# Performance work log

Measured on AMD Instinct MI355X. Metric: run time of the kernel, lower is better.

## Reference

```python
import jax, jax.numpy as jnp
import numpy as np

D_MODEL = 256
D_INNER = 512    # expand=2
D_STATE = 16
D_CONV = 4
DT_RANK = 16     # ceil(256/16)
N_BLOCKS = 4
EPS = 1e-5


def setup_inputs() -> dict:
    key = jax.random.key(0)
    ks = jax.random.split(key, 8)
    s = 0.02
    return {
        "x": jax.random.normal(ks[0], (1, 4, D_MODEL, 32, 32), jnp.float32),
        "norm_w": jnp.ones((N_BLOCKS, D_MODEL), jnp.float32),
        "norm_b": jnp.zeros((N_BLOCKS, D_MODEL), jnp.float32),
        "in_w": jax.random.normal(ks[1], (N_BLOCKS, 2 * D_INNER, D_MODEL), jnp.float32) * s,
        "conv_w": jax.random.normal(ks[2], (N_BLOCKS, D_INNER, D_CONV), jnp.float32) * s,
        "conv_b": jnp.zeros((N_BLOCKS, D_INNER), jnp.float32),
        "xproj_w": jax.random.normal(ks[3], (N_BLOCKS, DT_RANK + 2 * D_STATE, D_INNER), jnp.float32) * s,
        "dtproj_w": jax.random.normal(ks[4], (N_BLOCKS, D_INNER, DT_RANK), jnp.float32) * s,
        "dtproj_b": jax.random.normal(ks[5], (N_BLOCKS, D_INNER), jnp.float32) * s,
        "A_log": jnp.tile(jnp.log(jnp.arange(1, D_STATE + 1, dtype=jnp.float32))[None, None, :],
                          (N_BLOCKS, D_INNER, 1)),
        "Dp": jnp.ones((N_BLOCKS, D_INNER), jnp.float32),
        "out_w": jax.random.normal(ks[6], (N_BLOCKS, D_MODEL, D_INNER), jnp.float32) * s,
    }


def _layernorm(x, w, b):
    mu = jnp.mean(x, axis=-1, keepdims=True)
    var = jnp.var(x, axis=-1, keepdims=True)
    return (x - mu) / jnp.sqrt(var + EPS) * w + b


def _mamba(h, in_w, conv_w, conv_b, xproj_w, dtproj_w, dtproj_b, A_log, Dp, out_w):
    # h: (B, L, d_model)
    B, L, _ = h.shape
    xz = h @ in_w.T                                   # (B, L, 2*d_inner)
    x, z = jnp.split(xz, 2, axis=-1)
    # causal depthwise conv1d, kernel size D_CONV
    xp = jnp.pad(x, ((0, 0), (D_CONV - 1, 0), (0, 0)))
    xc = sum(xp[:, k:k + L, :] * conv_w[:, k] for k in range(D_CONV)) + conv_b
    x = jax.nn.silu(xc)                               # (B, L, d_inner)
    dbl = x @ xproj_w.T                               # (B, L, dt_rank + 2*d_state)
    dt = dbl[..., :DT_RANK]
    Bm = dbl[..., DT_RANK:DT_RANK + D_STATE]          # (B, L, n)
    Cm = dbl[..., DT_RANK + D_STATE:]                 # (B, L, n)
    dt = jax.nn.softplus(dt @ dtproj_w.T + dtproj_b)  # (B, L, d_inner)
    A = -jnp.exp(A_log)                               # (d_inner, n)
    dA = jnp.exp(dt[..., None] * A)                   # (B, L, d_inner, n)
    dBx = dt[..., None] * Bm[:, :, None, :] * x[..., None]

    def step(hprev, inp):
        dA_t, dBx_t, C_t = inp
        hcur = dA_t * hprev + dBx_t                   # (B, d_inner, n)
        return hcur, jnp.einsum('bdn,bn->bd', hcur, C_t)

    h0 = jnp.zeros((B, D_INNER, D_STATE), x.dtype)
    _, y = jax.lax.scan(step, h0, (dA.transpose(1, 0, 2, 3),
                                   dBx.transpose(1, 0, 2, 3),
                                   Cm.transpose(1, 0, 2)))
    y = y.transpose(1, 0, 2)                          # (B, L, d_inner)
    y = (y + Dp * x) * jax.nn.silu(z)
    return y @ out_w.T                                # (B, L, d_model)


def _forward(x, norm_w, norm_b, in_w, conv_w, conv_b, xproj_w, dtproj_w, dtproj_b, A_log, Dp, out_w):
    b, n, c, h, w = x.shape
    hs = x.reshape(b * n, c, h * w).transpose(0, 2, 1)  # (bn, hw, c)

    def blk(i, hidden, resid):
        resid = hidden if resid is None else resid + hidden
        hn = _layernorm(resid, norm_w[i], norm_b[i])
        out = _mamba(hn, in_w[i], conv_w[i], conv_b[i], xproj_w[i],
                     dtproj_w[i], dtproj_b[i], A_log[i], Dp[i], out_w[i])
        return out, resid

    res = None
    for i in range(2):  # pairs of (forward, backward-flipped) blocks
        hf, rf = blk(2 * i, hs, res)
        hb, rb = blk(2 * i + 1, hs[:, ::-1], None if res is None else res[:, ::-1])
        hs = hf + hb[:, ::-1]
        res = rf + rb[:, ::-1]
    res = res + hs
    return res.transpose(0, 2, 1).reshape(b, n, c, h, w)


def reference(x, norm_w, norm_b, in_w, conv_w, conv_b, xproj_w, dtproj_w, dtproj_b, A_log, Dp, out_w):
    return _forward(x, norm_w, norm_b, in_w, conv_w, conv_b, xproj_w,
                    dtproj_w, dtproj_b, A_log, Dp, out_w)
```

## Files before the change

kernel.cpp:

```cpp
#include <hip/hip_runtime.h>
#include <math.h>


__device__ __forceinline__ float sigmoidf_(float x){ return 1.f/(1.f+__expf(-x)); }
__device__ __forceinline__ short bf16_(float x){
  unsigned u = __float_as_uint(x);
  u += 0x7FFFu + ((u>>16)&1u);
  return (short)(u>>16);
}
__device__ __forceinline__ float f32_(short s){
  return __uint_as_float(((unsigned)(unsigned short)s)<<16);
}

using fragAB = __attribute__((ext_vector_type(8))) short;
using fragC  = __attribute__((ext_vector_type(4))) float;

__global__ __launch_bounds__(256) void k_transpose_in(const float* __restrict__ x, float* __restrict__ hs){
  __shared__ float tile[32][33];
  int b = blockIdx.z;
  int l0 = blockIdx.x*32, c0 = blockIdx.y*32;
  int tx = threadIdx.x, ty = threadIdx.y;
  #pragma unroll
  for (int j=0;j<32;j+=8)
    tile[ty+j][tx] = x[(size_t)b*262144 + (size_t)(c0+ty+j)*1024 + l0 + tx];
  __syncthreads();
  #pragma unroll
  for (int j=0;j<32;j+=8)
    hs[(size_t)b*262144 + (size_t)(l0+ty+j)*256 + (c0+tx)] = tile[tx][ty+j];
}

__global__ __launch_bounds__(256) void k_final(const float* __restrict__ racc, const float* __restrict__ hs, float* __restrict__ out){
  __shared__ float tile[32][33];
  int b = blockIdx.z;
  int l0 = blockIdx.x*32, c0 = blockIdx.y*32;
  int tx = threadIdx.x, ty = threadIdx.y;
  #pragma unroll
  for (int j=0;j<32;j+=8){
    size_t idx = (size_t)b*262144 + (size_t)(l0+ty+j)*256 + c0+tx;
    tile[ty+j][tx] = 2.f*racc[idx] + hs[idx];
  }
  __syncthreads();
  #pragma unroll
  for (int j=0;j<32;j+=8)
    out[(size_t)b*262144 + (size_t)(c0+ty+j)*1024 + l0+tx] = tile[tx][ty+j];
}

__global__ __launch_bounds__(256) void k_ln(const float* __restrict__ hs, float* __restrict__ racc, short* __restrict__ hn_f,
  const float* __restrict__ nw, const float* __restrict__ nb, int layer0, int first){
  int row = blockIdx.x, c = threadIdx.x;
  size_t idx = (size_t)row*256 + c;
  float r = hs[idx];
  if (!first) r += 2.f*racc[idx];
  racc[idx] = r;
  float s1=r, s2=r*r;
  #pragma unroll
  for (int o=32;o>=1;o>>=1){ s1+=__shfl_xor(s1,o); s2+=__shfl_xor(s2,o); }
  __shared__ float red[8];
  int wid=c>>6, lane=c&63;
  if (lane==0){ red[wid]=s1; red[4+wid]=s2; }
  __syncthreads();
  s1 = red[0]+red[1]+red[2]+red[3];
  s2 = red[4]+red[5]+red[6]+red[7];
  float mu = s1*(1.f/256.f);
  float var = s2*(1.f/256.f) - mu*mu;
  float inv = rsqrtf(var + 1e-5f);
  float nv = (r-mu)*inv;
  size_t fo = (((size_t)(row>>4)*32 + (c>>3))*16 + (row&15))*8 + (c&7);
  hn_f[fo]           = bf16_(nv*nw[layer0*256+c] + nb[layer0*256+c]);
  hn_f[1048576 + fo] = bf16_(nv*nw[(layer0+1)*256+c] + nb[(layer0+1)*256+c]);
}

__global__ __launch_bounds__(256) void k_wconv(
  const float* __restrict__ inw, const float* __restrict__ xpw,
  const float* __restrict__ dtw, const float* __restrict__ otw,
  short* __restrict__ f_inw, short* __restrict__ f_xpw,
  short* __restrict__ f_dtw, short* __restrict__ f_otw,
  short* __restrict__ dt_f)
{
  int which = blockIdx.y, layer = blockIdx.z;
  int idx = blockIdx.x*256 + threadIdx.x;
  if (which==4){
    if (layer) return;
    if (idx >= 131072) return;
    int st = idx >> 16, rem = idx & 65535;
    int mt = rem >> 8, kt2 = (rem>>7)&1, e = rem&127;
    dt_f[(size_t)st*131072 + ((size_t)(mt*4 + 2 + kt2))*128 + e] = 0;
    return;
  }
  const float* src; short* dst; int R,K,Kp;
  if (which==0){ src=inw; dst=f_inw; R=1024; K=256; Kp=256; }
  else if (which==1){ src=xpw; dst=f_xpw; R=48; K=512; Kp=512; }
  else if (which==2){ src=dtw; dst=f_dtw; R=512; K=16; Kp=32; }
  else { src=otw; dst=f_otw; R=256; K=512; Kp=512; }
  int per = (R>>4)*(Kp>>3)*128;
  if (idx >= per) return;
  int e = idx & 127, tile = idx >> 7;
  int nkt = Kp>>3;
  int kt = tile % nkt, rt = tile / nkt;
  int r = rt*16 + (e>>3), k = kt*8 + (e&7);
  float v = (k<K) ? src[((size_t)layer*R + r)*K + k] : 0.f;
  dst[(size_t)layer*per + idx] = bf16_(v);
}

__global__ __launch_bounds__(256) void k_mm(
  const short* __restrict__ Af, long sA,
  const short* __restrict__ Wf, long sW,
  const short* __restrict__ A2f, const short* __restrict__ W2f,
  float* __restrict__ Cb, long sC,
  const float* __restrict__ biasb, long sBias,
  int M, int N, int K, int ldc, int mode,
  short* __restrict__ aux1, long sAux1,
  short* __restrict__ aux2, long sAux2)
{
  int z = blockIdx.z;
  int tid = threadIdx.x;
  int lane = tid & 63, wid = tid >> 6;
  int wm = wid & 1, wn = wid >> 1;
  int K8 = K >> 3;
  int mt_base = blockIdx.y*8 + wm*4;
  int nt_base = blockIdx.x*4 + wn*2;
  int ncap = (N + 15) >> 4;
  const int loff = lane*8;
  fragC acc[4][2] = {};
  const short* Aps[2] = { Af + (size_t)z*sA, A2f };
  const short* Wps[2] = { Wf + (size_t)z*sW, W2f };
  int nseg = A2f ? 2 : 1;
  for (int sgi=0; sgi<nseg; ++sgi){
    const short* A = Aps[sgi];
    const short* W = Wps[sgi];
    for (int kt=0; kt<K8; kt+=4){
      fragAB a[4], b[2];
      #pragma unroll
      for (int i=0;i<4;++i)
        a[i] = *(const fragAB*)(A + ((size_t)(mt_base+i)*K8 + kt)*128 + loff);
      #pragma unroll
      for (int j=0;j<2;++j){
        int nt = nt_base + j; if (nt >= ncap) nt = ncap-1;
        b[j] = *(const fragAB*)(W + ((size_t)nt*K8 + kt)*128 + loff);
      }
      #pragma unroll
      for (int i=0;i<4;++i)
        #pragma unroll
        for (int j=0;j<2;++j)
          acc[i][j] = __builtin_amdgcn_mfma_f32_16x16x32_bf16(a[i], b[j], acc[i][j], 0,0,0);
    }
  }
  float* C = Cb ? Cb + (size_t)z*sC : nullptr;
  const float* bias = biasb ? biasb + (size_t)z*sBias : nullptr;
  int r0 = (lane>>4)*4;
  int cc = lane & 15;
  #pragma unroll
  for (int i=0;i<4;++i){
    int row = (mt_base+i)*16 + r0;
    #pragma unroll
    for (int j=0;j<2;++j){
      int col = (nt_base+j)*16 + cc;
      if (col < N){
        #pragma unroll
        for (int r=0;r<4;++r){
          float v = acc[i][j][r];
          if (bias) v += bias[col];
          if (mode==2){ v = (v > 20.f) ? v : log1pf(__expf(v)); }
          int rr = row + r;
          if (mode==3){
            if (col < 512) aux1[(size_t)z*sAux1 + (size_t)rr*512 + col] = bf16_(v);
            else           aux2[(size_t)z*sAux2 + (size_t)rr*512 + (col-512)] = bf16_(v);
          } else {
            C[(size_t)rr*ldc + col] = v;
            if (mode==1 && col < 16)
              aux1[(size_t)z*sAux1 + (((size_t)(rr>>4)*4 + (col>>3))*16 + (rr&15))*8 + (col&7)] = bf16_(v);
          }
        }
      }
    }
  }
}

__global__ __launch_bounds__(256) void k_conv(const short* __restrict__ xb, short* __restrict__ xc_f,
  const float* __restrict__ cw, const float* __restrict__ cb, int layer0){
  int idx = blockIdx.x*256 + threadIdx.x;
  int d = idx & 511;
  int t = (idx >> 9) & 1023;
  int sb = idx >> 19;
  int s = sb >> 2, b = sb & 3;
  int layer = layer0 + s;
  const float* w = cw + ((size_t)layer*512 + d)*4;
  float accv = cb[(size_t)layer*512 + d];
  const short* xp = xb + (size_t)s*2097152 + (size_t)b*1024*512 + d;
  if (s==0){
    #pragma unroll
    for (int k=0;k<4;++k){ int tt = t + k - 3; if (tt>=0) accv = fmaf(f32_(xp[(size_t)tt*512]), w[k], accv); }
  } else {
    #pragma unroll
    for (int k=0;k<4;++k){ int tt = t + 3 - k; if (tt<1024) accv = fmaf(f32_(xp[(size_t)tt*512]), w[k], accv); }
  }
  float v = accv * sigmoidf_(accv);
  int row = b*1024 + t;
  xc_f[(size_t)s*2097152 + (((size_t)(row>>4)*64 + (d>>3))*16 + (row&15))*8 + (d&7)] = bf16_(v);
}

#define NCHUNK 64
#define CSTEPS 16

__device__ __forceinline__ float ld_xc(const short* xcf, int row, int d){
  return f32_(xcf[(((size_t)(row>>4)*64 + (d>>3))*16 + (row&15))*8 + (d&7)]);
}

__global__ __launch_bounds__(256) void k_scan_a(
  const float* __restrict__ dtv, const short* __restrict__ xc_f,
  const float* __restrict__ dbl, const float* __restrict__ A_log,
  float* __restrict__ dtsum, float* __restrict__ hF, int layer0)
{
  int d = blockIdx.x*256 + threadIdx.x;
  int k = blockIdx.y;
  int sb = blockIdx.z;
  int s = sb >> 2, b = sb & 3;
  int layer = layer0 + s;
  float Av[16];
  #pragma unroll
  for (int n=0;n<16;++n) Av[n] = -__expf(A_log[((size_t)layer*512 + d)*16 + n]);
  const float* dt_p = dtv + (size_t)sb*524288 + d;
  const short* xcf = xc_f + (size_t)s*2097152;
  const float* bc_p = dbl + (size_t)sb*49152;
  float h[16];
  #pragma unroll
  for (int n=0;n<16;++n) h[n] = 0.f;
  float ssum = 0.f;
  int u0 = k*CSTEPS;
  #pragma unroll
  for (int i=0;i<CSTEPS;++i){
    int u = u0 + i;
    int t = s ? (1023 - u) : u;
    int row = b*1024 + t;
    float dtval = dt_p[(size_t)t*512];
    float xv = ld_xc(xcf, row, d);
    const float4* bp = (const float4*)(bc_p + (size_t)t*48 + 16);
    float4 B0 = bp[0], B1 = bp[1], B2 = bp[2], B3 = bp[3];
    float Bv[16] = {B0.x,B0.y,B0.z,B0.w,B1.x,B1.y,B1.z,B1.w,
                    B2.x,B2.y,B2.z,B2.w,B3.x,B3.y,B3.z,B3.w};
    float w = dtval * xv;
    ssum += dtval;
    #pragma unroll
    for (int n=0;n<16;++n)
      h[n] = fmaf(__expf(dtval*Av[n]), h[n], w*Bv[n]);
  }
  size_t base = (size_t)(sb*NCHUNK + k)*512 + d;
  dtsum[base] = ssum;
  float4* hp = (float4*)(hF + base*16);
  #pragma unroll
  for (int q=0;q<4;++q) hp[q] = make_float4(h[4*q],h[4*q+1],h[4*q+2],h[4*q+3]);
}

__global__ __launch_bounds__(256) void k_scan_c(
  const float* __restrict__ dtsum, float* __restrict__ hF,
  const float* __restrict__ A_log, int layer0)
{
  int gid = blockIdx.x*256 + threadIdx.x;
  int sb = gid >> 13;
  int d = (gid >> 4) & 511;
  int n = gid & 15;
  int layer = layer0 + (sb >> 2);
  float Av = -__expf(A_log[((size_t)layer*512 + d)*16 + n]);
  float hrun = 0.f;
  #pragma unroll 8
  for (int k=0;k<NCHUNK;++k){
    size_t base = (size_t)(sb*NCHUNK + k)*512 + d;
    float a = __expf(Av * dtsum[base]);
    float hf = hF[base*16 + n];
    hF[base*16 + n] = hrun;
    hrun = fmaf(a, hrun, hf);
  }
}

__global__ __launch_bounds__(256) void k_scan_b(
  const float* __restrict__ dtv, const short* __restrict__ xc_f, const short* __restrict__ zb,
  const float* __restrict__ dbl, const float* __restrict__ A_log, const float* __restrict__ Dp,
  const float* __restrict__ h0p, short* __restrict__ y_f, int layer0)
{
  int d = blockIdx.x*256 + threadIdx.x;
  int k = blockIdx.y;
  int sb = blockIdx.z;
  int s = sb >> 2, b = sb & 3;
  int layer = layer0 + s;
  float Av[16];
  #pragma unroll
  for (int n=0;n<16;++n) Av[n] = -__expf(A_log[((size_t)layer*512 + d)*16 + n]);
  float Dv = Dp[(size_t)layer*512 + d];
  const float* dt_p = dtv + (size_t)sb*524288 + d;
  const short* xcf = xc_f + (size_t)s*2097152;
  const short* z_p = zb + (size_t)s*2097152 + (size_t)b*1024*512 + d;
  const float* bc_p = dbl + (size_t)sb*49152;
  size_t base = (size_t)(sb*NCHUNK + k)*512 + d;
  float h[16];
  const float4* hp = (const float4*)(h0p + base*16);
  #pragma unroll
  for (int q=0;q<4;++q){
    float4 v = hp[q];
    h[4*q]=v.x; h[4*q+1]=v.y; h[4*q+2]=v.z; h[4*q+3]=v.w;
  }
  short* yo = y_f + (size_t)s*2097152;
  int u0 = k*CSTEPS;
  #pragma unroll
  for (int i=0;i<CSTEPS;++i){
    int u = u0 + i;
    int t = s ? (1023 - u) : u;
    int row = b*1024 + t;
    float dtval = dt_p[(size_t)t*512];
    float xv = ld_xc(xcf, row, d);
    const float4* bp = (const float4*)(bc_p + (size_t)t*48 + 16);
    float4 B0 = bp[0], B1 = bp[1], B2 = bp[2], B3 = bp[3];
    float4 C0 = bp[4], C1 = bp[5], C2 = bp[6], C3 = bp[7];
    float Bv[16] = {B0.x,B0.y,B0.z,B0.w,B1.x,B1.y,B1.z,B1.w,
                    B2.x,B2.y,B2.z,B2.w,B3.x,B3.y,B3.z,B3.w};
    float Cv[16] = {C0.x,C0.y,C0.z,C0.w,C1.x,C1.y,C1.z,C1.w,
                    C2.x,C2.y,C2.z,C2.w,C3.x,C3.y,C3.z,C3.w};
    float w = dtval * xv;
    float y = 0.f;
    #pragma unroll
    for (int n=0;n<16;++n){
      h[n] = fmaf(__expf(dtval*Av[n]), h[n], w*Bv[n]);
      y = fmaf(h[n], Cv[n], y);
    }
    float zv = f32_(z_p[(size_t)t*512]);
    float yv = (y + Dv*xv) * (zv*sigmoidf_(zv));
    yo[(((size_t)(row>>4)*64 + (d>>3))*16 + (row&15))*8 + (d&7)] = bf16_(yv);
  }
}

extern "C" void kernel_launch(void* const* d_in, const int* in_sizes, int n_in,
                              void* d_out, int out_size, void* d_ws, size_t ws_size,
                              hipStream_t stream) {
  const float* x        = (const float*)d_in[0];
  const float* norm_w   = (const float*)d_in[1];
  const float* norm_b   = (const float*)d_in[2];
  const float* in_w     = (const float*)d_in[3];
  const float* conv_w   = (const float*)d_in[4];
  const float* conv_b   = (const float*)d_in[5];
  const float* xproj_w  = (const float*)d_in[6];
  const float* dtproj_w = (const float*)d_in[7];
  const float* dtproj_b = (const float*)d_in[8];
  const float* A_log    = (const float*)d_in[9];
  const float* Dp       = (const float*)d_in[10];
  const float* out_w    = (const float*)d_in[11];
  float* out = (float*)d_out;
  float* ws = (float*)d_ws;

  float* hs    = ws;
  float* racc  = ws + 1048576;
  short* hn_f  = (short*)(ws + 2097152);
  short* xb    = (short*)(ws + 3145728);
  short* zb    = (short*)(ws + 5242880);
  short* xc_f  = (short*)(ws + 7340032);
  short* y_f   = (short*)(ws + 9437184);
  float* dbl   = ws + 11534336;
  float* dtv   = ws + 12058624;
  short* dt_f  = (short*)(ws + 16252928);
  float* dtsum = ws + 16384000;
  float* hF    = ws + 16646144;
  short* w_inw = (short*)(ws + 20840448);
  short* w_xp  = w_inw + 1048576;
  short* w_dt  = w_xp + 98304;
  short* w_out = w_dt + 65536;

  k_wconv<<<dim3(1024,5,4), 256, 0, stream>>>(in_w, xproj_w, dtproj_w, out_w,
      w_inw, w_xp, w_dt, w_out, dt_f);
  k_transpose_in<<<dim3(32,8,4), dim3(32,8), 0, stream>>>(x, hs);

  for (int it=0; it<2; ++it){
    int layer0 = 2*it;
    k_ln<<<4096, 256, 0, stream>>>(hs, racc, hn_f, norm_w, norm_b, layer0, it==0 ? 1 : 0);
    k_mm<<<dim3(16,32,2), 256, 0, stream>>>(hn_f, 1048576L, w_inw + (size_t)layer0*262144, 262144L,
        nullptr, nullptr, nullptr, 0L, nullptr, 0L, 4096, 1024, 256, 0, 3,
        xb, 2097152L, zb, 2097152L);
    k_conv<<<16384, 256, 0, stream>>>(xb, xc_f, conv_w, conv_b, layer0);
    k_mm<<<dim3(1,32,2), 256, 0, stream>>>(xc_f, 2097152L, w_xp + (size_t)layer0*24576, 24576L,
        nullptr, nullptr, dbl, 196608L, nullptr, 0L, 4096, 48, 512, 48, 1,
        dt_f, 131072L, nullptr, 0L);
    k_mm<<<dim3(8,32,2), 256, 0, stream>>>(dt_f, 131072L, w_dt + (size_t)layer0*16384, 16384L,
        nullptr, nullptr, dtv, 2097152L, dtproj_b + (size_t)layer0*512, 512L, 4096, 512, 32, 512, 2,
        nullptr, 0L, nullptr, 0L);
    k_scan_a<<<dim3(2,NCHUNK,8), 256, 0, stream>>>(dtv, xc_f, dbl, A_log, dtsum, hF, layer0);
    k_scan_c<<<256, 256, 0, stream>>>(dtsum, hF, A_log, layer0);
    k_scan_b<<<dim3(2,NCHUNK,8), 256, 0, stream>>>(dtv, xc_f, zb, dbl, A_log, Dp, hF, y_f, layer0);
    k_mm<<<dim3(4,32,1), 256, 0, stream>>>(y_f, 0L, w_out + (size_t)layer0*131072, 0L,
        y_f + 2097152, w_out + (size_t)(layer0+1)*131072, hs, 0L, nullptr, 0L,
        4096, 256, 512, 256, 0, nullptr, 0L, nullptr, 0L);
  }
  k_final<<<dim3(32,8,4), dim3(32,8), 0, stream>>>(racc, hs, out);
}
```

Before: 458.2 us.

## Fuse x/dt projections, widen GEMM tiles, parallelize chunk scan, compact weight conversion

The x-projection and dt-projection GEMMs are fused into one kernel that keeps the dt slice in LDS and applies bias and softplus in place, so the dt_f round trip and one launch go away. The generic GEMM becomes k_mm4 with 4x4 MFMA tiles per wave, which halves the grid and raises per-wave reuse. The sequential cross-chunk scan in k_scan_c becomes a parallel warp-shuffle prefix scan over chunks per (d, sb) block. Weight conversion uses a compact 1D grid with no idle blocks. In exchange, the larger tiles raise register pressure and the in_proj grid drops to 512 blocks, and the scan now assumes NCHUNK equals 64.

```diff
diff --git a/kernel.cpp b/kernel.cpp
--- a/kernel.cpp
+++ b/kernel.cpp
@@ -74,26 +74,20 @@
   const float* __restrict__ inw, const float* __restrict__ xpw,
   const float* __restrict__ dtw, const float* __restrict__ otw,
   short* __restrict__ f_inw, short* __restrict__ f_xpw,
-  short* __restrict__ f_dtw, short* __restrict__ f_otw,
-  short* __restrict__ dt_f)
-{
-  int which = blockIdx.y, layer = blockIdx.z;
-  int idx = blockIdx.x*256 + threadIdx.x;
-  if (which==4){
-    if (layer) return;
-    if (idx >= 131072) return;
-    int st = idx >> 16, rem = idx & 65535;
-    int mt = rem >> 8, kt2 = (rem>>7)&1, e = rem&127;
-    dt_f[(size_t)st*131072 + ((size_t)(mt*4 + 2 + kt2))*128 + e] = 0;
-    return;
-  }
+  short* __restrict__ f_dtw, short* __restrict__ f_otw)
+{
+  int b = blockIdx.x, tid = threadIdx.x;
+  int which, layer, idx;
+  if (b < 4096){ which=0; layer=b>>10; idx=((b&1023)<<8)+tid; }
+  else if (b < 4480){ int r=b-4096; which=1; layer=r/96;  idx=(r%96)*256+tid; }
+  else if (b < 4736){ int r=b-4480; which=2; layer=r>>6;  idx=(r&63)*256+tid; }
+  else              { int r=b-4736; which=3; layer=r>>9;  idx=(r&511)*256+tid; }
   const float* src; short* dst; int R,K,Kp;
   if (which==0){ src=inw; dst=f_inw; R=1024; K=256; Kp=256; }
   else if (which==1){ src=xpw; dst=f_xpw; R=48; K=512; Kp=512; }
   else if (which==2){ src=dtw; dst=f_dtw; R=512; K=16; Kp=32; }
   else { src=otw; dst=f_otw; R=256; K=512; Kp=512; }
   int per = (R>>4)*(Kp>>3)*128;
-  if (idx >= per) return;
   int e = idx & 127, tile = idx >> 7;
   int nkt = Kp>>3;
   int kt = tile % nkt, rt = tile / nkt;
@@ -102,13 +96,12 @@
   dst[(size_t)layer*per + idx] = bf16_(v);
 }
 
-__global__ __launch_bounds__(256) void k_mm(
+__global__ __launch_bounds__(256) void k_mm4(
   const short* __restrict__ Af, long sA,
   const short* __restrict__ Wf, long sW,
   const short* __restrict__ A2f, const short* __restrict__ W2f,
   float* __restrict__ Cb, long sC,
-  const float* __restrict__ biasb, long sBias,
-  int M, int N, int K, int ldc, int mode,
+  int K, int ldc, int mode,
   short* __restrict__ aux1, long sAux1,
   short* __restrict__ aux2, long sAux2)
 {
@@ -118,10 +111,9 @@
   int wm = wid & 1, wn = wid >> 1;
   int K8 = K >> 3;
   int mt_base = blockIdx.y*8 + wm*4;
-  int nt_base = blockIdx.x*4 + wn*2;
-  int ncap = (N + 15) >> 4;
+  int nt_base = blockIdx.x*8 + wn*4;
   const int loff = lane*8;
-  fragC acc[4][2] = {};
+  fragC acc[4][4] = {};
   const short* Aps[2] = { Af + (size_t)z*sA, A2f };
   const short* Wps[2] = { Wf + (size_t)z*sW, W2f };
   int nseg = A2f ? 2 : 1;
@@ -129,46 +121,125 @@
     const short* A = Aps[sgi];
     const short* W = Wps[sgi];
     for (int kt=0; kt<K8; kt+=4){
-      fragAB a[4], b[2];
+      fragAB a[4], b[4];
       #pragma unroll
       for (int i=0;i<4;++i)
         a[i] = *(const fragAB*)(A + ((size_t)(mt_base+i)*K8 + kt)*128 + loff);
       #pragma unroll
-      for (int j=0;j<2;++j){
-        int nt = nt_base + j; if (nt >= ncap) nt = ncap-1;
-        b[j] = *(const fragAB*)(W + ((size_t)nt*K8 + kt)*128 + loff);
-      }
+      for (int j=0;j<4;++j)
+        b[j] = *(const fragAB*)(W + ((size_t)(nt_base+j)*K8 + kt)*128 + loff);
       #pragma unroll
       for (int i=0;i<4;++i)
         #pragma unroll
-        for (int j=0;j<2;++j)
+        for (int j=0;j<4;++j)
           acc[i][j] = __builtin_amdgcn_mfma_f32_16x16x32_bf16(a[i], b[j], acc[i][j], 0,0,0);
     }
   }
   float* C = Cb ? Cb + (size_t)z*sC : nullptr;
-  const float* bias = biasb ? biasb + (size_t)z*sBias : nullptr;
   int r0 = (lane>>4)*4;
   int cc = lane & 15;
   #pragma unroll
   for (int i=0;i<4;++i){
     int row = (mt_base+i)*16 + r0;
     #pragma unroll
-    for (int j=0;j<2;++j){
+    for (int j=0;j<4;++j){
       int col = (nt_base+j)*16 + cc;
-      if (col < N){
+      #pragma unroll
+      for (int r=0;r<4;++r){
+        float v = acc[i][j][r];
+        int rr = row + r;
+        if (mode==3){
+          if (col < 512) aux1[(size_t)z*sAux1 + (size_t)rr*512 + col] = bf16_(v);
+          else           aux2[(size_t)z*sAux2 + (size_t)rr*512 + (col-512)] = bf16_(v);
+        } else {
+          C[(size_t)rr*ldc + col] = v;
+        }
+      }
+    }
+  }
+}
+
+__global__ __launch_bounds__(256) void k_xpdt(
+  const short* __restrict__ xc_f, const short* __restrict__ wxp,
+  const short* __restrict__ wdt, const float* __restrict__ dtb,
+  float* __restrict__ dbl, float* __restrict__ dtv, int layer0)
+{
+  __shared__ short dt_lds[32][24];
+  int z = blockIdx.y;
+  int by = blockIdx.x;
+  int layer = layer0 + z;
+  int tid = threadIdx.x, lane = tid & 63, wn = tid >> 6;
+  const short* A = xc_f + (size_t)z*2097152;
+  const short* W = wxp + (size_t)layer*24576;
+  int mt0 = by*2;
+  const int loff = lane*8;
+  int r0 = (lane>>4)*4, cc = lane & 15;
+  {
+    fragC acc[2] = {};
+    int nt = wn < 3 ? wn : 2;
+    for (int kt=0; kt<64; kt+=4){
+      fragAB a0 = *(const fragAB*)(A + ((size_t)(mt0+0)*64 + kt)*128 + loff);
+      fragAB a1 = *(const fragAB*)(A + ((size_t)(mt0+1)*64 + kt)*128 + loff);
+      fragAB b  = *(const fragAB*)(W + ((size_t)nt*64 + kt)*128 + loff);
+      acc[0] = __builtin_amdgcn_mfma_f32_16x16x32_bf16(a0, b, acc[0], 0,0,0);
+      acc[1] = __builtin_amdgcn_mfma_f32_16x16x32_bf16(a1, b, acc[1], 0,0,0);
+    }
+    int col = nt*16 + cc;
+    #pragma unroll
+    for (int i=0;i<2;++i){
+      int lr = i*16 + r0;
+      int grow = by*32 + lr;
+      #pragma unroll
+      for (int r=0;r<4;++r){
+        float v = acc[i][r];
+        if (wn==1 || wn==2)
+          dbl[(size_t)z*196608 + (size_t)(grow+r)*48 + col] = v;
+        if (wn==0)
+          dt_lds[lr+r][cc] = bf16_(v);
+      }
+    }
+  }
+  __syncthreads();
+  {
+    float* dto = dtv + (size_t)z*2097152;
+    const float* bias = dtb + (size_t)layer*512;
+    const short* WD = wdt + (size_t)layer*16384;
+    int kq = lane >> 4;
+    fragAB a2[2];
+    #pragma unroll
+    for (int i=0;i<2;++i){
+      fragAB t = {};
+      if (kq < 2){
         #pragma unroll
-        for (int r=0;r<4;++r){
-          float v = acc[i][j][r];
-          if (bias) v += bias[col];
-          if (mode==2){ v = (v > 20.f) ? v : log1pf(__expf(v)); }
-          int rr = row + r;
-          if (mode==3){
-            if (col < 512) aux1[(size_t)z*sAux1 + (size_t)rr*512 + col] = bf16_(v);
-            else           aux2[(size_t)z*sAux2 + (size_t)rr*512 + (col-512)] = bf16_(v);
-          } else {
-            C[(size_t)rr*ldc + col] = v;
-            if (mode==1 && col < 16)
-              aux1[(size_t)z*sAux1 + (((size_t)(rr>>4)*4 + (col>>3))*16 + (rr&15))*8 + (col&7)] = bf16_(v);
+        for (int j=0;j<8;++j) t[j] = dt_lds[i*16 + (lane&15)][kq*8 + j];
+      }
+      a2[i] = t;
+    }
+    #pragma unroll
+    for (int c2=0;c2<2;++c2){
+      fragC acc2[2][4] = {};
+      fragAB b2[4];
+      #pragma unroll
+      for (int j=0;j<4;++j){
+        int ntj = wn*8 + c2*4 + j;
+        b2[j] = *(const fragAB*)(WD + ((size_t)ntj*4)*128 + loff);
+      }
+      #pragma unroll
+      for (int i=0;i<2;++i)
+        #pragma unroll
+        for (int j=0;j<4;++j)
+          acc2[i][j] = __builtin_amdgcn_mfma_f32_16x16x32_bf16(a2[i], b2[j], acc2[i][j], 0,0,0);
+      #pragma unroll
+      for (int i=0;i<2;++i){
+        int grow = by*32 + i*16 + r0;
+        #pragma unroll
+        for (int j=0;j<4;++j){
+          int col2 = (wn*8 + c2*4 + j)*16 + cc;
+          #pragma unroll
+          for (int r=0;r<4;++r){
+            float v = acc2[i][j][r] + bias[col2];
+            v = (v > 20.f) ? v : log1pf(__expf(v));
+            dto[(size_t)(grow+r)*512 + col2] = v;
           }
         }
       }
@@ -255,20 +326,41 @@
   const float* __restrict__ dtsum, float* __restrict__ hF,
   const float* __restrict__ A_log, int layer0)
 {
-  int gid = blockIdx.x*256 + threadIdx.x;
-  int sb = gid >> 13;
-  int d = (gid >> 4) & 511;
-  int n = gid & 15;
+  __shared__ float tile[64][17];
+  __shared__ float ds[64];
+  int d = blockIdx.x, sb = blockIdx.y;
+  int tid = threadIdx.x, lane = tid & 63, w = tid >> 6;
   int layer = layer0 + (sb >> 2);
-  float Av = -__expf(A_log[((size_t)layer*512 + d)*16 + n]);
-  float hrun = 0.f;
-  #pragma unroll 8
-  for (int k=0;k<NCHUNK;++k){
-    size_t base = (size_t)(sb*NCHUNK + k)*512 + d;
-    float a = __expf(Av * dtsum[base]);
-    float hf = hF[base*16 + n];
-    hF[base*16 + n] = hrun;
-    hrun = fmaf(a, hrun, hf);
+  size_t base = (size_t)sb*64*8192 + (size_t)d*16;
+  {
+    int k = tid >> 2, n0 = (tid & 3)*4;
+    float4 v = *(const float4*)(hF + base + (size_t)k*8192 + n0);
+    tile[k][n0+0]=v.x; tile[k][n0+1]=v.y; tile[k][n0+2]=v.z; tile[k][n0+3]=v.w;
+  }
+  if (tid < 64) ds[tid] = dtsum[((size_t)sb*64 + tid)*512 + d];
+  __syncthreads();
+  float dsk = ds[lane];
+  #pragma unroll
+  for (int p=0;p<4;++p){
+    int n = p*4 + w;
+    float Av = -__expf(A_log[((size_t)layer*512 + d)*16 + n]);
+    float a = __expf(Av * dsk);
+    float h = tile[lane][n];
+    #pragma unroll
+    for (int o=1;o<64;o<<=1){
+      float au = __shfl_up(a, o);
+      float hu = __shfl_up(h, o);
+      if (lane >= o){ h = fmaf(a, hu, h); a *= au; }
+    }
+    float h0 = __shfl_up(h, 1);
+    if (lane == 0) h0 = 0.f;
+    tile[lane][n] = h0;
+  }
+  __syncthreads();
+  {
+    int k = tid >> 2, n0 = (tid & 3)*4;
+    float4 v = make_float4(tile[k][n0], tile[k][n0+1], tile[k][n0+2], tile[k][n0+3]);
+    *(float4*)(hF + base + (size_t)k*8192 + n0) = v;
   }
 }
 
@@ -354,37 +446,29 @@
   short* y_f   = (short*)(ws + 9437184);
   float* dbl   = ws + 11534336;
   float* dtv   = ws + 12058624;
-  short* dt_f  = (short*)(ws + 16252928);
-  float* dtsum = ws + 16384000;
-  float* hF    = ws + 16646144;
-  short* w_inw = (short*)(ws + 20840448);
+  float* dtsum = ws + 16252928;
+  float* hF    = ws + 16515072;
+  short* w_inw = (short*)(ws + 20709376);
   short* w_xp  = w_inw + 1048576;
   short* w_dt  = w_xp + 98304;
   short* w_out = w_dt + 65536;
 
-  k_wconv<<<dim3(1024,5,4), 256, 0, stream>>>(in_w, xproj_w, dtproj_w, out_w,
-      w_inw, w_xp, w_dt, w_out, dt_f);
+  k_wconv<<<6784, 256, 0, stream>>>(in_w, xproj_w, dtproj_w, out_w, w_inw, w_xp, w_dt, w_out);
   k_transpose_in<<<dim3(32,8,4), dim3(32,8), 0, stream>>>(x, hs);
 
   for (int it=0; it<2; ++it){
     int layer0 = 2*it;
     k_ln<<<4096, 256, 0, stream>>>(hs, racc, hn_f, norm_w, norm_b, layer0, it==0 ? 1 : 0);
-    k_mm<<<dim3(16,32,2), 256, 0, stream>>>(hn_f, 1048576L, w_inw + (size_t)layer0*262144, 262144L,
-        nullptr, nullptr, nullptr, 0L, nullptr, 0L, 4096, 1024, 256, 0, 3,
-        xb, 2097152L, zb, 2097152L);
+    k_mm4<<<dim3(8,32,2), 256, 0, stream>>>(hn_f, 1048576L, w_inw + (size_t)layer0*262144, 262144L,
+        nullptr, nullptr, nullptr, 0L, 256, 0, 3, xb, 2097152L, zb, 2097152L);
     k_conv<<<16384, 256, 0, stream>>>(xb, xc_f, conv_w, conv_b, layer0);
-    k_mm<<<dim3(1,32,2), 256, 0, stream>>>(xc_f, 2097152L, w_xp + (size_t)layer0*24576, 24576L,
-        nullptr, nullptr, dbl, 196608L, nullptr, 0L, 4096, 48, 512, 48, 1,
-        dt_f, 131072L, nullptr, 0L);
-    k_mm<<<dim3(8,32,2), 256, 0, stream>>>(dt_f, 131072L, w_dt + (size_t)layer0*16384, 16384L,
-        nullptr, nullptr, dtv, 2097152L, dtproj_b + (size_t)layer0*512, 512L, 4096, 512, 32, 512, 2,
+    k_xpdt<<<dim3(128,2), 256, 0, stream>>>(xc_f, w_xp, w_dt, dtproj_b, dbl, dtv, layer0);
+    k_scan_a<<<dim3(2,NCHUNK,8), 256, 0, stream>>>(dtv, xc_f, dbl, A_log, dtsum, hF, layer0);
+    k_scan_c<<<dim3(512,8), 256, 0, stream>>>(dtsum, hF, A_log, layer0);
+    k_scan_b<<<dim3(2,NCHUNK,8), 256, 0, stream>>>(dtv, xc_f, zb, dbl, A_log, Dp, hF, y_f, layer0);
+    k_mm4<<<dim3(2,32,1), 256, 0, stream>>>(y_f, 0L, w_out + (size_t)layer0*131072, 0L,
+        y_f + 2097152, w_out + (size_t)(layer0+1)*131072, hs, 0L, 512, 256, 0,
         nullptr, 0L, nullptr, 0L);
-    k_scan_a<<<dim3(2,NCHUNK,8), 256, 0, stream>>>(dtv, xc_f, dbl, A_log, dtsum, hF, layer0);
-    k_scan_c<<<256, 256, 0, stream>>>(dtsum, hF, A_log, layer0);
-    k_scan_b<<<dim3(2,NCHUNK,8), 256, 0, stream>>>(dtv, xc_f, zb, dbl, A_log, Dp, hF, y_f, layer0);
-    k_mm<<<dim3(4,32,1), 256, 0, stream>>>(y_f, 0L, w_out + (size_t)layer0*131072, 0L,
-        y_f + 2097152, w_out + (size_t)(layer0+1)*131072, hs, 0L, nullptr, 0L,
-        4096, 256, 512, 256, 0, nullptr, 0L, nullptr, 0L);
   }
   k_final<<<dim3(32,8,4), dim3(32,8), 0, stream>>>(racc, hs, out);
 }
```

New measurement: 446.3 us. 1.03x faster.
